# Performance work log

Hardware: AMD Instinct MI355X
Metric: run time of the kernel (lower is better)

## Reference

```python
import jax, jax.numpy as jnp
import numpy as np

# --- Clifford algebra constants for a 4D Euclidean space (MULTIVECTOR_DIM = 16) ---
# grades 0..4 have dims (1,4,6,4,1); component index -> grade:
GRADE_OF = np.array([0] + [1]*4 + [2]*6 + [3]*4 + [4], dtype=np.int64)  # [16]
# reversion sign per grade k: (-1)^{k(k-1)/2}
_REV_PER_GRADE = np.array([1.0, 1.0, -1.0, -1.0, 1.0], dtype=np.float32)
REVERSION = jnp.asarray(_REV_PER_GRADE[GRADE_OF])            # [16]
# scalar part of geometric product of orthonormal basis blades: diag of reversion signs
SCALAR_TABLE = jnp.asarray(np.diag(_REV_PER_GRADE[GRADE_OF]).astype(np.float32))  # [16,16]
SCALE = 1.0 / np.sqrt(16.0)

B, S, H, M = 4, 2048, 8, 16


def _block_masks():
    block = (GRADE_OF[:, None] == GRADE_OF[None, :]).astype(np.float32)  # [16,16]
    bias = ((GRADE_OF == 0) | (GRADE_OF == 4)).astype(np.float32)        # [16]
    return jnp.asarray(block), jnp.asarray(bias)


def setup_inputs() -> dict:
    key = jax.random.key(0)
    ks = jax.random.split(key, 10)
    block, bias = _block_masks()
    def w_in(k):   # [16, H, 16], zero outside grade blocks (j -> i within same grade)
        return jax.random.normal(k, (M, H, M), jnp.float32) * 0.1 * block[:, None, :]
    def b_in(k):   # [H, 16], only grade-0 / grade-4 components have bias
        return jax.random.normal(k, (H, M), jnp.float32) * 0.1 * bias[None, :]
    x = jax.random.normal(ks[0], (B, S, M), jnp.float32)
    return {
        "x": x,
        "wq": w_in(ks[1]), "bq": b_in(ks[2]),
        "wk": w_in(ks[3]), "bk": b_in(ks[4]),
        "wv": w_in(ks[5]), "bv": b_in(ks[6]),
        "wo": jax.random.normal(ks[7], (H, M, M), jnp.float32) * 0.1 * block[None, :, :],
        "bo": jax.random.normal(ks[8], (M,), jnp.float32) * 0.1 * bias,
    }


def reference(x, wq, bq, wk, bk, wv, bv, wo, bo):
    # per-grade Q/K/V projections, packed as block-sparse linears over 16 components
    q = jnp.einsum('bsj,jhi->bhsi', x, wq) + bq[None, :, None, :]  # [B,H,S,16]
    k = jnp.einsum('bsj,jhi->bhsi', x, wk) + bk[None, :, None, :]
    v = jnp.einsum('bsj,jhi->bhsi', x, wv) + bv[None, :, None, :]
    k_rev = k * REVERSION[None, None, None, :]
    # scalar part of geometric product <Q * reverse(K)>_0 via fixed bilinear table
    scores = jnp.einsum('bhqi,bhkj,ij->bhqk', q, k_rev, SCALAR_TABLE) * SCALE
    attn = jax.nn.softmax(scores, axis=-1)                         # [B,H,S,S]
    head = jnp.einsum('bhqk,bhki->bhqi', attn, v)                  # [B,H,S,16]
    # per-grade output projections (block over heads x grade components)
    out = jnp.einsum('bhqj,hji->bqi', head, wo) + bo               # [B,S,16]
    return out
```

## Files before the change

### kernel.cpp

```cpp
#include <hip/hip_runtime.h>

#define BB 4
#define SS 2048
#define HH 8
#define MM 16

#define QSCALE 0.36067376022224085f

typedef __attribute__((ext_vector_type(8)))  short short8;
typedef __attribute__((ext_vector_type(4)))  int   int4v;
typedef __attribute__((ext_vector_type(4)))  float f32x4;
typedef __attribute__((ext_vector_type(16))) float f32x16;

static constexpr size_t NQKV = (size_t)BB * HH * SS * MM;

__device__ __forceinline__ int pk_bf16(float lo, float hi) {
    int r;
    asm("v_cvt_pk_bf16_f32 %0, %1, %2" : "=v"(r) : "v"(lo), "v"(hi));
    return r;
}

__device__ __forceinline__ void proj16(const float xr[16], const float* __restrict__ w,
                                       const float* __restrict__ bias, int h, float out[16]) {
#pragma unroll
    for (int i = 0; i < 16; i++) out[i] = bias[(h << 4) + i];
#pragma unroll
    for (int j = 0; j < 16; j++) {
        float xj = xr[j];
        const float* wr = w + (((j * HH) + h) << 4);
#pragma unroll
        for (int i = 0; i < 16; i++) out[i] = fmaf(xj, wr[i], out[i]);
    }
}

__device__ __forceinline__ void pack_store(ushort* dst, const float o[16], float scale) {
    int4v w0, w1;
#pragma unroll
    for (int j = 0; j < 4; j++) w0[j] = pk_bf16(o[2*j] * scale,     o[2*j+1] * scale);
#pragma unroll
    for (int j = 0; j < 4; j++) w1[j] = pk_bf16(o[8+2*j] * scale,   o[8+2*j+1] * scale);
    int4v* p = (int4v*)dst;
    p[0] = w0; p[1] = w1;
}

__global__ __launch_bounds__(256) void proj_kernel(
    const float* __restrict__ x,
    const float* __restrict__ wq, const float* __restrict__ bq,
    const float* __restrict__ wk, const float* __restrict__ bk,
    const float* __restrict__ wv, const float* __restrict__ bv,
    ushort* __restrict__ qb, ushort* __restrict__ kb, ushort* __restrict__ vb)
{
    int h  = blockIdx.x >> 5;
    int bs = ((blockIdx.x & 31) << 8) + threadIdx.x;
    int b  = bs >> 11;

    float xr[16];
    const float4* x4 = (const float4*)(x + (size_t)bs * MM);
#pragma unroll
    for (int j = 0; j < 4; j++) {
        float4 t = x4[j];
        xr[j*4+0] = t.x; xr[j*4+1] = t.y; xr[j*4+2] = t.z; xr[j*4+3] = t.w;
    }

    size_t orow = (((size_t)(b * HH + h) * SS) + (bs & 2047)) * MM;
    float o[16];

    proj16(xr, wq, bq, h, o);  pack_store(qb + orow, o, QSCALE);
    proj16(xr, wk, bk, h, o);  pack_store(kb + orow, o, 1.0f);
    proj16(xr, wv, bv, h, o);  pack_store(vb + orow, o, 1.0f);
}

__global__ __launch_bounds__(512, 4) void attn_kernel(
    const ushort* __restrict__ qb, const ushort* __restrict__ kb,
    const ushort* __restrict__ vb, float* __restrict__ hb)
{
    __shared__ ushort Kl[2][2][128 * 24];
    __shared__ ushort Vl[2][2][32 * 136];

    int tid = threadIdx.x;
    int grp = tid >> 8;
    int t8  = tid & 255;
    int nb = ((blockIdx.x & 7) << 6) | (blockIdx.x >> 3);
    int bh = nb >> 4, qt = nb & 15;
    size_t base = (size_t)bh * SS * MM;
    const ushort* Qg = qb + base;
    const ushort* Kg = kb + base;
    const ushort* Vg = vb + base;

    int lane = tid & 63;
    int wid4 = (tid >> 6) & 3;
    int n = lane & 31, c = lane >> 5;
    int q = qt * 128 + wid4 * 32 + n;

    for (int i = t8; i < 136; i += 256) {
        Vl[grp][0][16 * 136 + i] = 0x3F80;
        Vl[grp][0][20 * 136 + i] = 0x3F80;
        Vl[grp][1][16 * 136 + i] = 0x3F80;
        Vl[grp][1][20 * 136 + i] = 0x3F80;
    }

    short8 qf = *(const short8*)(Qg + (size_t)q * MM + c * 8);

    int srow = t8 >> 1, shalf = t8 & 1;
    int vr = lane & 31;

    {
        int kt = grp * 8;
        int4v kw = *(const int4v*)(Kg + (size_t)((kt << 7) + srow) * MM + shalf * 8);
        int4v vw = *(const int4v*)(Vg + (size_t)((kt << 7) + srow) * MM + shalf * 8);
        *(int4v*)&Kl[grp][0][srow * 24 + shalf * 8] = kw;
        union { int4v v; ushort s[8]; } vu; vu.v = vw;
#pragma unroll
        for (int j = 0; j < 8; j++) Vl[grp][0][(8 * shalf + j) * 136 + srow] = vu.s[j];
    }
    __syncthreads();

    f32x16 oacc = 0;
    const f32x16 zacc = 0;

    for (int it = 0; it < 8; it++) {
        int cur = it & 1;
        const ushort* Klds = Kl[grp][cur];
        const ushort* Vt   = Vl[grp][cur];

        int4v kw, vw;
        if (it != 7) {
            int kt = grp * 8 + it + 1;
            kw = *(const int4v*)(Kg + (size_t)((kt << 7) + srow) * MM + shalf * 8);
            vw = *(const int4v*)(Vg + (size_t)((kt << 7) + srow) * MM + shalf * 8);
        }

#pragma unroll
        for (int sub = 0; sub < 4; sub++) {
            short8 kf = *(const short8*)&Klds[(sub * 32 + n) * 24 + c * 8];
            f32x16 s = __builtin_amdgcn_mfma_f32_32x32x16_bf16(kf, qf, zacc, 0, 0, 0);

            float pv[16];
#pragma unroll
            for (int r = 0; r < 16; r++) pv[r] = __builtin_amdgcn_exp2f(s[r]);

            int a0 = pk_bf16(pv[0],  pv[1]);
            int a1 = pk_bf16(pv[2],  pv[3]);
            int a2 = pk_bf16(pv[4],  pv[5]);
            int a3 = pk_bf16(pv[6],  pv[7]);
            int a4 = pk_bf16(pv[8],  pv[9]);
            int a5 = pk_bf16(pv[10], pv[11]);
            int a6 = pk_bf16(pv[12], pv[13]);
            int a7 = pk_bf16(pv[14], pv[15]);

            int w0 = a0, w2 = a2;
            asm("v_permlane32_swap_b32 %0, %1" : "+v"(w0), "+v"(w2));
            int w1 = a1, w3 = a3;
            asm("v_permlane32_swap_b32 %0, %1" : "+v"(w1), "+v"(w3));
            int u0 = a4, u2 = a6;
            asm("v_permlane32_swap_b32 %0, %1" : "+v"(u0), "+v"(u2));
            int u1 = a5, u3 = a7;
            asm("v_permlane32_swap_b32 %0, %1" : "+v"(u1), "+v"(u3));

            int4v bi1 = {w0, w1, w2, w3};
            int4v bi2 = {u0, u1, u2, u3};
            short8 B1 = __builtin_bit_cast(short8, bi1);
            short8 B2 = __builtin_bit_cast(short8, bi2);

            short8 vf1 = *(const short8*)&Vt[vr * 136 + sub * 32 + c * 8];
            short8 vf2 = *(const short8*)&Vt[vr * 136 + sub * 32 + 16 + c * 8];
            oacc = __builtin_amdgcn_mfma_f32_32x32x16_bf16(vf1, B1, oacc, 0, 0, 0);
            oacc = __builtin_amdgcn_mfma_f32_32x32x16_bf16(vf2, B2, oacc, 0, 0, 0);
        }

        if (it != 7) {
            *(int4v*)&Kl[grp][cur ^ 1][srow * 24 + shalf * 8] = kw;
            union { int4v v; ushort s[8]; } vu; vu.v = vw;
#pragma unroll
            for (int j = 0; j < 8; j++) Vl[grp][cur ^ 1][(8 * shalf + j) * 136 + srow] = vu.s[j];
        }
        __syncthreads();
    }

    float* mg = (float*)&Kl[0][0][0];
    int ql = wid4 * 32 + n;

    if (grp == 1) {
#pragma unroll
        for (int j = 0; j < 4; j++) mg[ql * 18 + 4 * c + j]     = oacc[j];
#pragma unroll
        for (int j = 0; j < 4; j++) mg[ql * 18 + 8 + 4 * c + j] = oacc[4 + j];
        mg[ql * 18 + 16 + c] = oacc[8];
    }
    __syncthreads();
    if (grp == 0) {
        float inv = 1.0f / (oacc[8] + mg[ql * 18 + 16 + c]);

        float* orow = hb + base + (size_t)q * MM;
        f32x4 o0, o1;
#pragma unroll
        for (int j = 0; j < 4; j++)
            o0[j] = (oacc[j]     + mg[ql * 18 + 4 * c + j])     * inv;
#pragma unroll
        for (int j = 0; j < 4; j++)
            o1[j] = (oacc[4 + j] + mg[ql * 18 + 8 + 4 * c + j]) * inv;
        *(f32x4*)(orow + 4 * c) = o0;
        *(f32x4*)(orow + 8 + 4 * c) = o1;
    }
}

__global__ __launch_bounds__(128) void outproj_kernel(
    const float* __restrict__ hb, const float* __restrict__ wo,
    const float* __restrict__ bo, float* __restrict__ out)
{
    int tid = threadIdx.x;
    int row = blockIdx.x * 64 + (tid >> 1);
    int hh = tid & 1;
    int b = row >> 11, s = row & 2047;

    float acc[16];
#pragma unroll
    for (int i = 0; i < 16; i++) acc[i] = 0.0f;

    for (int hi = 0; hi < 4; hi++) {
        int h = hh * 4 + hi;
        const float* hr = hb + ((size_t)(b * 8 + h) * SS + s) * MM;
        float hv[16];
        const f32x4* h4 = (const f32x4*)hr;
#pragma unroll
        for (int j = 0; j < 4; j++) {
            f32x4 tv = h4[j];
            hv[j*4+0] = tv[0]; hv[j*4+1] = tv[1]; hv[j*4+2] = tv[2]; hv[j*4+3] = tv[3];
        }
#pragma unroll
        for (int j = 0; j < 16; j++) {
            float hj = hv[j];
            const float* wr = wo + (((h << 4) + j) << 4);
#pragma unroll
            for (int i = 0; i < 16; i++) acc[i] = fmaf(hj, wr[i], acc[i]);
        }
    }

#pragma unroll
    for (int i = 0; i < 16; i++) acc[i] += __shfl_xor(acc[i], 1);

    if (hh == 0) {
        float* op = out + (size_t)row * MM;
#pragma unroll
        for (int j = 0; j < 4; j++) {
            f32x4 v = {acc[4*j+0] + bo[4*j+0], acc[4*j+1] + bo[4*j+1],
                       acc[4*j+2] + bo[4*j+2], acc[4*j+3] + bo[4*j+3]};
            *(f32x4*)(op + 4*j) = v;
        }
    }
}

extern "C" void kernel_launch(void* const* d_in, const int* in_sizes, int n_in,
                              void* d_out, int out_size, void* d_ws, size_t ws_size,
                              hipStream_t stream) {
    const float* x  = (const float*)d_in[0];
    const float* wq = (const float*)d_in[1];
    const float* bq = (const float*)d_in[2];
    const float* wk = (const float*)d_in[3];
    const float* bk = (const float*)d_in[4];
    const float* wv = (const float*)d_in[5];
    const float* bv = (const float*)d_in[6];
    const float* wo = (const float*)d_in[7];
    const float* bo = (const float*)d_in[8];
    float* out = (float*)d_out;

    ushort* qb = (ushort*)d_ws;
    ushort* kb = qb + NQKV;
    ushort* vb = kb + NQKV;
    float*  hb = (float*)(vb + NQKV);

    proj_kernel<<<256, 256, 0, stream>>>(x, wq, bq, wk, bk, wv, bv, qb, kb, vb);
    attn_kernel<<<512, 512, 0, stream>>>(qb, kb, vb, hb);
    outproj_kernel<<<128, 128, 0, stream>>>(hb, wo, bo, out);
}
```

Baseline: 43.21 us.

## Split keys across four waves per 32-query block with per-wave LDS staging

The attention kernel moves from 512-thread blocks (128 queries, two key halves) to 256-thread blocks covering 32 queries. Each of the four waves handles a quarter of the keys and a four-way LDS reduction combines the partial results. K fragments are now read straight from global memory instead of LDS, and each wave transposes its own V tile into private LDS, so no block barriers are needed inside the loop. This trades block-wide synchronisation and shared K staging for more blocks and more global K traffic, plus a larger final reduction.

Measured after the change: 44.68 us. 3.4% more time.

```diff
diff --git a/kernel.cpp b/kernel.cpp
--- a/kernel.cpp
+++ b/kernel.cpp
@@ -70,69 +70,55 @@
     proj16(xr, wv, bv, h, o);  pack_store(vb + orow, o, 1.0f);
 }
 
-__global__ __launch_bounds__(512, 4) void attn_kernel(
+__global__ __launch_bounds__(256, 8) void attn_kernel(
     const ushort* __restrict__ qb, const ushort* __restrict__ kb,
     const ushort* __restrict__ vb, float* __restrict__ hb)
 {
-    __shared__ ushort Kl[2][2][128 * 24];
-    __shared__ ushort Vl[2][2][32 * 136];
+    __shared__ ushort Vl[4][32 * 72];
 
     int tid = threadIdx.x;
-    int grp = tid >> 8;
-    int t8  = tid & 255;
-    int nb = ((blockIdx.x & 7) << 6) | (blockIdx.x >> 3);
-    int bh = nb >> 4, qt = nb & 15;
+    int w = tid >> 6;
+    int lane = tid & 63;
+    int n = lane & 31, c = lane >> 5;
+
+    int nb = ((blockIdx.x & 7) << 8) | (blockIdx.x >> 3);
+    int bh = nb >> 6, qt = nb & 63;
     size_t base = (size_t)bh * SS * MM;
     const ushort* Qg = qb + base;
     const ushort* Kg = kb + base;
     const ushort* Vg = vb + base;
 
-    int lane = tid & 63;
-    int wid4 = (tid >> 6) & 3;
-    int n = lane & 31, c = lane >> 5;
-    int q = qt * 128 + wid4 * 32 + n;
-
-    for (int i = t8; i < 136; i += 256) {
-        Vl[grp][0][16 * 136 + i] = 0x3F80;
-        Vl[grp][0][20 * 136 + i] = 0x3F80;
-        Vl[grp][1][16 * 136 + i] = 0x3F80;
-        Vl[grp][1][20 * 136 + i] = 0x3F80;
-    }
-
+    int q = qt * 32 + n;
     short8 qf = *(const short8*)(Qg + (size_t)q * MM + c * 8);
 
-    int srow = t8 >> 1, shalf = t8 & 1;
-    int vr = lane & 31;
-
-    {
-        int kt = grp * 8;
-        int4v kw = *(const int4v*)(Kg + (size_t)((kt << 7) + srow) * MM + shalf * 8);
-        int4v vw = *(const int4v*)(Vg + (size_t)((kt << 7) + srow) * MM + shalf * 8);
-        *(int4v*)&Kl[grp][0][srow * 24 + shalf * 8] = kw;
-        union { int4v v; ushort s[8]; } vu; vu.v = vw;
-#pragma unroll
-        for (int j = 0; j < 8; j++) Vl[grp][0][(8 * shalf + j) * 136 + srow] = vu.s[j];
-    }
-    __syncthreads();
+    ushort* Vt = Vl[w];
+    for (int i = lane; i < 72; i += 64) {
+        Vt[16 * 72 + i] = 0x3F80;
+        Vt[20 * 72 + i] = 0x3F80;
+    }
 
     f32x16 oacc = 0;
     const f32x16 zacc = 0;
 
-    for (int it = 0; it < 8; it++) {
-        int cur = it & 1;
-        const ushort* Klds = Kl[grp][cur];
-        const ushort* Vt   = Vl[grp][cur];
-
-        int4v kw, vw;
-        if (it != 7) {
-            int kt = grp * 8 + it + 1;
-            kw = *(const int4v*)(Kg + (size_t)((kt << 7) + srow) * MM + shalf * 8);
-            vw = *(const int4v*)(Vg + (size_t)((kt << 7) + srow) * MM + shalf * 8);
-        }
-
-#pragma unroll
-        for (int sub = 0; sub < 4; sub++) {
-            short8 kf = *(const short8*)&Klds[(sub * 32 + n) * 24 + c * 8];
+    int k0 = w * 512;
+    int4v vwa = *(const int4v*)(Vg + (size_t)(k0 + lane) * MM);
+    int4v vwb = *(const int4v*)(Vg + (size_t)(k0 + lane) * MM + 8);
+
+    for (int t = 0; t < 8; t++) {
+        union { int4v v; ushort s[8]; } ua, ub;
+        ua.v = vwa; ub.v = vwb;
+#pragma unroll
+        for (int j = 0; j < 8; j++) Vt[j * 72 + lane] = ua.s[j];
+#pragma unroll
+        for (int j = 0; j < 8; j++) Vt[(8 + j) * 72 + lane] = ub.s[j];
+        if (t != 7) {
+            vwa = *(const int4v*)(Vg + (size_t)(k0 + (t + 1) * 64 + lane) * MM);
+            vwb = *(const int4v*)(Vg + (size_t)(k0 + (t + 1) * 64 + lane) * MM + 8);
+        }
+
+#pragma unroll
+        for (int sub = 0; sub < 2; sub++) {
+            short8 kf = *(const short8*)(Kg + (size_t)(k0 + t * 64 + sub * 32 + n) * MM + c * 8);
             f32x16 s = __builtin_amdgcn_mfma_f32_32x32x16_bf16(kf, qf, zacc, 0, 0, 0);
 
             float pv[16];
@@ -162,45 +148,45 @@
             short8 B1 = __builtin_bit_cast(short8, bi1);
             short8 B2 = __builtin_bit_cast(short8, bi2);
 
-            short8 vf1 = *(const short8*)&Vt[vr * 136 + sub * 32 + c * 8];
-            short8 vf2 = *(const short8*)&Vt[vr * 136 + sub * 32 + 16 + c * 8];
+            int vr = lane & 31;
+            short8 vf1 = *(const short8*)&Vt[vr * 72 + sub * 32 + c * 8];
+            short8 vf2 = *(const short8*)&Vt[vr * 72 + sub * 32 + 16 + c * 8];
             oacc = __builtin_amdgcn_mfma_f32_32x32x16_bf16(vf1, B1, oacc, 0, 0, 0);
             oacc = __builtin_amdgcn_mfma_f32_32x32x16_bf16(vf2, B2, oacc, 0, 0, 0);
         }
-
-        if (it != 7) {
-            *(int4v*)&Kl[grp][cur ^ 1][srow * 24 + shalf * 8] = kw;
-            union { int4v v; ushort s[8]; } vu; vu.v = vw;
-#pragma unroll
-            for (int j = 0; j < 8; j++) Vl[grp][cur ^ 1][(8 * shalf + j) * 136 + srow] = vu.s[j];
-        }
-        __syncthreads();
-    }
-
-    float* mg = (float*)&Kl[0][0][0];
-    int ql = wid4 * 32 + n;
-
-    if (grp == 1) {
-#pragma unroll
-        for (int j = 0; j < 4; j++) mg[ql * 18 + 4 * c + j]     = oacc[j];
-#pragma unroll
-        for (int j = 0; j < 4; j++) mg[ql * 18 + 8 + 4 * c + j] = oacc[4 + j];
-        mg[ql * 18 + 16 + c] = oacc[8];
-    }
+    }
+
     __syncthreads();
-    if (grp == 0) {
-        float inv = 1.0f / (oacc[8] + mg[ql * 18 + 16 + c]);
-
+    float* mg = (float*)&Vl[0][0];
+    if (w != 0) {
+        float* dst = mg + (size_t)(w - 1) * 576 + n * 18;
+#pragma unroll
+        for (int j = 0; j < 4; j++) dst[4 * c + j]     = oacc[j];
+#pragma unroll
+        for (int j = 0; j < 4; j++) dst[8 + 4 * c + j] = oacc[4 + j];
+        dst[16 + c] = oacc[8];
+    }
+    __syncthreads();
+    if (w == 0) {
+        float l = oacc[8];
+        float o0[4], o1[4];
+#pragma unroll
+        for (int j = 0; j < 4; j++) { o0[j] = oacc[j]; o1[j] = oacc[4 + j]; }
+#pragma unroll
+        for (int p = 0; p < 3; p++) {
+            const float* src = mg + (size_t)p * 576 + n * 18;
+#pragma unroll
+            for (int j = 0; j < 4; j++) o0[j] += src[4 * c + j];
+#pragma unroll
+            for (int j = 0; j < 4; j++) o1[j] += src[8 + 4 * c + j];
+            l += src[16 + c];
+        }
+        float inv = 1.0f / l;
         float* orow = hb + base + (size_t)q * MM;
-        f32x4 o0, o1;
-#pragma unroll
-        for (int j = 0; j < 4; j++)
-            o0[j] = (oacc[j]     + mg[ql * 18 + 4 * c + j])     * inv;
-#pragma unroll
-        for (int j = 0; j < 4; j++)
-            o1[j] = (oacc[4 + j] + mg[ql * 18 + 8 + 4 * c + j]) * inv;
-        *(f32x4*)(orow + 4 * c) = o0;
-        *(f32x4*)(orow + 8 + 4 * c) = o1;
+        f32x4 v0 = {o0[0] * inv, o0[1] * inv, o0[2] * inv, o0[3] * inv};
+        f32x4 v1 = {o1[0] * inv, o1[1] * inv, o1[2] * inv, o1[3] * inv};
+        *(f32x4*)(orow + 4 * c) = v0;
+        *(f32x4*)(orow + 8 + 4 * c) = v1;
     }
 }
 
@@ -270,6 +256,6 @@
     float*  hb = (float*)(vb + NQKV);
 
     proj_kernel<<<256, 256, 0, stream>>>(x, wq, bq, wk, bk, wv, bv, qb, kb, vb);
-    attn_kernel<<<512, 512, 0, stream>>>(qb, kb, vb, hb);
+    attn_kernel<<<2048, 256, 0, stream>>>(qb, kb, vb, hb);
     outproj_kernel<<<128, 128, 0, stream>>>(hb, wo, bo, out);
 }
```
